# Optimization experiments

Measured on AMD Instinct MI355X. Metric: run time of the kernel, lower is better.

The kernel has to match this reference:

```python
import jax, jax.numpy as jnp
import numpy as np


def _safe_div(x, y):
    # avoid NaNs in branches that are masked out by jnp.where
    return x / jnp.where(jnp.abs(y) < 1e-12, 1.0, y)


def _closest_point_region(p, a, b, c):
    """Ericson closest-point-on-triangle, vectorized.
    p: [B,n,1,3]; a,b,c: [B,1,m,3] -> (dist2 [B,n,m], region [B,n,m] int32).
    Region codes: 0=vertA 1=vertB 2=vertC 3=edgeAB 4=edgeAC 5=edgeBC 6=face.
    """
    ab = b - a; ac = c - a; cb = c - b
    ap = p - a; bp = p - b; cp = p - c
    d1 = (ab * ap).sum(-1); d2 = (ac * ap).sum(-1)
    d3 = (ab * bp).sum(-1); d4 = (ac * bp).sum(-1)
    d5 = (ab * cp).sum(-1); d6 = (ac * cp).sum(-1)
    vc = d1 * d4 - d3 * d2
    vb = d5 * d2 - d1 * d6
    va = d3 * d6 - d5 * d4

    # candidate closest points per region
    v_ab = jnp.clip(_safe_div(d1, d1 - d3), 0.0, 1.0)
    v_ac = jnp.clip(_safe_div(d2, d2 - d6), 0.0, 1.0)
    v_bc = jnp.clip(_safe_div(d4 - d3, (d4 - d3) + (d5 - d6)), 0.0, 1.0)
    denom = va + vb + vc
    v_f = _safe_div(vb, denom); w_f = _safe_div(vc, denom)

    q_face = a + v_f[..., None] * ab + w_f[..., None] * ac
    q_ab = a + v_ab[..., None] * ab
    q_ac = a + v_ac[..., None] * ac
    q_bc = b + v_bc[..., None] * cb

    # region conditions (Ericson priority: a, b, ab, c, ac, bc, face)
    cond_a = (d1 <= 0) & (d2 <= 0)
    cond_b = (d3 >= 0) & (d4 <= d3)
    cond_ab = (vc <= 0) & (d1 >= 0) & (d3 <= 0)
    cond_c = (d6 >= 0) & (d5 <= d6)
    cond_ac = (vb <= 0) & (d2 >= 0) & (d6 <= 0)
    cond_bc = (va <= 0) & (d4 - d3 >= 0) & (d5 - d6 >= 0)

    def sel(cond, qc, code, q, region):
        q = jnp.where(cond[..., None], qc, q)
        region = jnp.where(cond, code, region)
        return q, region

    # apply lowest priority first so higher-priority regions overwrite
    q = q_face
    region = jnp.full(q.shape[:-1], 6, dtype=jnp.int32)
    q, region = sel(cond_bc, q_bc, 5, q, region)
    q, region = sel(cond_ac, q_ac, 4, q, region)
    q, region = sel(cond_c, c, 2, q, region)
    q, region = sel(cond_ab, q_ab, 3, q, region)
    q, region = sel(cond_b, b, 1, q, region)
    q, region = sel(cond_a, a, 0, q, region)

    diff = p - q
    dist2 = (diff * diff).sum(-1)  # squared distance, as in chamfer-style kernels
    return dist2, region


def setup_inputs() -> dict:
    key = jax.random.key(0)
    k1, k2, k3, k4 = jax.random.split(key, 4)
    B, n, m = 4, 4096, 512
    xyz1 = jax.random.normal(k1, (B, n, 3), dtype=jnp.float32)
    tri1 = jax.random.normal(k2, (B, m, 3), dtype=jnp.float32)
    tri2 = jax.random.normal(k3, (B, m, 3), dtype=jnp.float32)
    tri3 = jax.random.normal(k4, (B, m, 3), dtype=jnp.float32)
    return {"xyz1": xyz1, "tri1": tri1, "tri2": tri2, "tri3": tri3}


def reference(xyz1, tri1, tri2, tri3):
    p = xyz1[:, :, None, :]       # [B,n,1,3]
    a = tri1[:, None, :, :]       # [B,1,m,3]
    b = tri2[:, None, :, :]
    c = tri3[:, None, :, :]
    dist2, region = _closest_point_region(p, a, b, c)  # [B,n,m]
    index = jnp.argmin(dist2, axis=-1).astype(jnp.int32)            # [B,n]
    dist = jnp.min(dist2, axis=-1)                                  # [B,n]
    point = jnp.take_along_axis(region, index[..., None].astype(jnp.int64), axis=-1)[..., 0]
    return dist, point, index
```

## Files before the change

### kernel.cpp

```cpp
#include <hip/hip_runtime.h>
#include <math.h>

#define BB 4
#define NN 4096
#define MM 512
#define PTS 16
#define NPT 2
#define CHUNKS 32
#define MCHUNK (MM / CHUNKS)
#define TPB 512

__device__ __forceinline__ float safercp(float y) {
    float yy = (fabsf(y) < 1e-12f) ? 1.0f : y;
    return __builtin_amdgcn_rcpf(yy);
}

__device__ __forceinline__ float safediv(float x, float y) {
    float yy = (fabsf(y) < 1e-12f) ? 1.0f : y;
    return x / yy;
}

__device__ __forceinline__ float clip01(float x) {
    return fminf(fmaxf(x, 0.0f), 1.0f);
}

__device__ void exact_pair(float px, float py, float pz,
                           float ax, float ay, float az,
                           float bx, float by, float bz,
                           float cx, float cy, float cz,
                           float* dist2_out, int* reg_out) {
#pragma clang fp contract(off)
    const float abx = bx-ax, aby = by-ay, abz = bz-az;
    const float acx = cx-ax, acy = cy-ay, acz = cz-az;
    const float cbx = cx-bx, cby = cy-by, cbz = cz-bz;
    const float apx = px-ax, apy = py-ay, apz = pz-az;
    const float bpx = px-bx, bpy = py-by, bpz = pz-bz;
    const float cpx = px-cx, cpy = py-cy, cpz = pz-cz;

    const float d1 = abx*apx + aby*apy + abz*apz;
    const float d2 = acx*apx + acy*apy + acz*apz;
    const float d3 = abx*bpx + aby*bpy + abz*bpz;
    const float d4 = acx*bpx + acy*bpy + acz*bpz;
    const float d5 = abx*cpx + aby*cpy + abz*cpz;
    const float d6 = acx*cpx + acy*cpy + acz*cpz;

    const float vc = d1*d4 - d3*d2;
    const float vb = d5*d2 - d1*d6;
    const float va = d3*d6 - d5*d4;

    const float v_ab = clip01(safediv(d1, d1 - d3));
    const float v_ac = clip01(safediv(d2, d2 - d6));
    const float t43 = d4 - d3;
    const float t56 = d5 - d6;
    const float v_bc = clip01(safediv(t43, t43 + t56));
    const float denom = va + vb + vc;
    const float v_f = safediv(vb, denom);
    const float w_f = safediv(vc, denom);

    float qx = ax + v_f*abx + w_f*acx;
    float qy = ay + v_f*aby + w_f*acy;
    float qz = az + v_f*abz + w_f*acz;
    int reg = 6;
    const bool c_bc = (va <= 0.0f) && (t43 >= 0.0f) && (t56 >= 0.0f);
    if (c_bc) { qx = bx + v_bc*cbx; qy = by + v_bc*cby; qz = bz + v_bc*cbz; reg = 5; }
    const bool c_ac = (vb <= 0.0f) && (d2 >= 0.0f) && (d6 <= 0.0f);
    if (c_ac) { qx = ax + v_ac*acx; qy = ay + v_ac*acy; qz = az + v_ac*acz; reg = 4; }
    const bool c_c = (d6 >= 0.0f) && (d5 <= d6);
    if (c_c) { qx = cx; qy = cy; qz = cz; reg = 2; }
    const bool c_ab = (vc <= 0.0f) && (d1 >= 0.0f) && (d3 <= 0.0f);
    if (c_ab) { qx = ax + v_ab*abx; qy = ay + v_ab*aby; qz = az + v_ab*abz; reg = 3; }
    const bool c_b = (d3 >= 0.0f) && (d4 <= d3);
    if (c_b) { qx = bx; qy = by; qz = bz; reg = 1; }
    const bool c_a = (d1 <= 0.0f) && (d2 <= 0.0f);
    if (c_a) { qx = ax; qy = ay; qz = az; reg = 0; }

    const float dx = px - qx;
    const float dy = py - qy;
    const float dz = pz - qz;
    *dist2_out = dx*dx + dy*dy + dz*dz;
    *reg_out = reg;
}

__global__ __launch_bounds__(TPB) void tridist_kernel(
    const float* __restrict__ xyz1, const float* __restrict__ tri1,
    const float* __restrict__ tri2, const float* __restrict__ tri3,
    float* __restrict__ out)
{
    __shared__ float4 sT[MM * 7 + MM / 16];
    __shared__ float  sPd[NPT][128];
    __shared__ int    sPj[NPT][128];

    const int t  = threadIdx.x;
    const int b  = blockIdx.x >> 7;
    const int pb = blockIdx.x & 127;
    const int pt = t & (PTS - 1);
    const int ch = t >> 4;

    {
        const int jj = t;
        const float* g1 = tri1 + ((size_t)b * MM + jj) * 3;
        const float* g2 = tri2 + ((size_t)b * MM + jj) * 3;
        const float* g3 = tri3 + ((size_t)b * MM + jj) * 3;
        const float ax = g1[0], ay = g1[1], az = g1[2];
        const float bx = g2[0], by = g2[1], bz = g2[2];
        const float cx = g3[0], cy = g3[1], cz = g3[2];
        const float abx = bx-ax, aby = by-ay, abz = bz-az;
        const float acx = cx-ax, acy = cy-ay, acz = cz-az;
        const float cbx = cx-bx, cby = cy-by, cbz = cz-bz;
        const float aba  = fmaf(abz, az, fmaf(aby, ay, abx*ax));
        const float abb  = fmaf(abz, bz, fmaf(aby, by, abx*bx));
        const float abc_ = fmaf(abz, cz, fmaf(aby, cy, abx*cx));
        const float aca  = fmaf(acz, az, fmaf(acy, ay, acx*ax));
        const float acb_ = fmaf(acz, bz, fmaf(acy, by, acx*bx));
        const float acc_ = fmaf(acz, cz, fmaf(acy, cy, acx*cx));
        const float ab2  = fmaf(abz, abz, fmaf(aby, aby, abx*abx));
        const float ac2  = fmaf(acz, acz, fmaf(acy, acy, acx*acx));
        const float cb2  = fmaf(cbz, cbz, fmaf(cby, cby, cbx*cbx));
        const float abac = fmaf(abz, acz, fmaf(aby, acy, abx*acx));
        const float gdet = fmaf(ab2, ac2, -(abac*abac));
        const int base = jj * 7 + (jj >> 4);
        sT[base + 0] = make_float4(ax, ay, az, safercp(gdet));
        sT[base + 1] = make_float4(abx, aby, abz, safercp(ab2));
        sT[base + 2] = make_float4(acx, acy, acz, safercp(ac2));
        sT[base + 3] = make_float4(cbx, cby, cbz, safercp(cb2));
        sT[base + 4] = make_float4(aba, abb, abc_, cx);
        sT[base + 5] = make_float4(aca, acb_, acc_, cy);
        sT[base + 6] = make_float4(bx, by, bz, cz);
    }
    __syncthreads();

    float px[NPT], py[NPT], pz[NPT];
#pragma unroll
    for (int np = 0; np < NPT; ++np) {
        const int gi = b * NN + pb * 32 + np * PTS + pt;
        px[np] = xyz1[gi*3 + 0];
        py[np] = xyz1[gi*3 + 1];
        pz[np] = xyz1[gi*3 + 2];
    }

    float bestd[NPT] = {INFINITY, INFINITY};
    int   bestj[NPT] = {0, 0};

    for (int i = 0; i < MCHUNK; ++i) {
        const int j = ch * MCHUNK + i;
        const int base = j * 7 + ch;
        const float4 r0 = sT[base + 0];
        const float4 r1 = sT[base + 1];
        const float4 r2 = sT[base + 2];
        const float4 r3 = sT[base + 3];
        const float4 r4 = sT[base + 4];
        const float4 r5 = sT[base + 5];
        const float ax = r0.x, ay = r0.y, az = r0.z, rden = r0.w;
        const float abx = r1.x, aby = r1.y, abz = r1.z, rab2 = r1.w;
        const float acx = r2.x, acy = r2.y, acz = r2.z, rac2 = r2.w;
        const float cbx = r3.x, cby = r3.y, cbz = r3.z, rcb2 = r3.w;
        const float aba = r4.x, abb = r4.y, abc_ = r4.z;
        const float aca = r5.x, acb_ = r5.y, acc_ = r5.z;

#pragma unroll
        for (int np = 0; np < NPT; ++np) {
            const float s1 = fmaf(abz, pz[np], fmaf(aby, py[np], abx*px[np]));
            const float s2 = fmaf(acz, pz[np], fmaf(acy, py[np], acx*px[np]));
            const float d1 = s1 - aba, d3 = s1 - abb, d5 = s1 - abc_;
            const float d2 = s2 - aca, d4 = s2 - acb_, d6 = s2 - acc_;

            const float vc = fmaf(d1, d4, -(d3*d2));
            const float vb = fmaf(d5, d2, -(d1*d6));
            const float va = fmaf(d3, d6, -(d5*d4));
            const float t43 = d4 - d3;

            const float v_ab = clip01(d1 * rab2);
            const float v_ac = clip01(d2 * rac2);
            const float v_bc = clip01(t43 * rcb2);
            const float v_f = vb * rden;
            const float w_f = vc * rden;

            const float apx = px[np] - ax, apy = py[np] - ay, apz = pz[np] - az;
            const float bpx = apx - abx, bpy = apy - aby, bpz = apz - abz;

            float ex = fmaf(-v_ab, abx, apx), ey = fmaf(-v_ab, aby, apy), ez = fmaf(-v_ab, abz, apz);
            const float dAB = fmaf(ez, ez, fmaf(ey, ey, ex*ex));
            ex = fmaf(-v_ac, acx, apx); ey = fmaf(-v_ac, acy, apy); ez = fmaf(-v_ac, acz, apz);
            const float dAC = fmaf(ez, ez, fmaf(ey, ey, ex*ex));
            ex = fmaf(-v_bc, cbx, bpx); ey = fmaf(-v_bc, cby, bpy); ez = fmaf(-v_bc, cbz, bpz);
            const float dBC = fmaf(ez, ez, fmaf(ey, ey, ex*ex));
            ex = fmaf(-w_f, acx, fmaf(-v_f, abx, apx));
            ey = fmaf(-w_f, acy, fmaf(-v_f, aby, apy));
            ez = fmaf(-w_f, acz, fmaf(-v_f, abz, apz));
            const float dF = fmaf(ez, ez, fmaf(ey, ey, ex*ex));

            const bool inside = (va >= 0.0f) && (vb >= 0.0f) && (vc >= 0.0f);
            const float dseg = fminf(fminf(dAB, dAC), dBC);
            const float dist2 = inside ? dF : dseg;

            if (dist2 < bestd[np]) { bestd[np] = dist2; bestj[np] = j; }
        }
    }

#pragma unroll
    for (int np = 0; np < NPT; ++np) {
        for (int off = 16; off <= 32; off <<= 1) {
            const float od = __shfl_xor(bestd[np], off, 64);
            const int   oj = __shfl_xor(bestj[np], off, 64);
            if (od < bestd[np] || (od == bestd[np] && oj < bestj[np])) {
                bestd[np] = od; bestj[np] = oj;
            }
        }
    }
    const int lane = t & 63;
    const int w    = t >> 6;
    if (lane < PTS) {
#pragma unroll
        for (int np = 0; np < NPT; ++np) {
            sPd[np][w * PTS + lane] = bestd[np];
            sPj[np][w * PTS + lane] = bestj[np];
        }
    }
    __syncthreads();

    if (t < 32) {
        const int np = t >> 4;
        const int p  = t & 15;
        float bd = INFINITY; int bj = 0;
        for (int k = 0; k < 8; ++k) {
            const float dk = sPd[np][k * PTS + p];
            const int   jk = sPj[np][k * PTS + p];
            if (dk < bd || (dk == bd && jk < bj)) { bd = dk; bj = jk; }
        }
        const int base = bj * 7 + (bj >> 4);
        const float4 r0 = sT[base + 0];
        const float4 r4 = sT[base + 4];
        const float4 r5 = sT[base + 5];
        const float4 r6 = sT[base + 6];
        const int gidx = b * NN + pb * 32 + t;
        float dist2; int reg;
        exact_pair(xyz1[gidx*3+0], xyz1[gidx*3+1], xyz1[gidx*3+2],
                   r0.x, r0.y, r0.z,
                   r6.x, r6.y, r6.z,
                   r4.w, r5.w, r6.w,
                   &dist2, &reg);
        out[gidx]             = dist2;
        out[BB*NN + gidx]     = (float)reg;
        out[2*BB*NN + gidx]   = (float)bj;
    }
}

extern "C" void kernel_launch(void* const* d_in, const int* in_sizes, int n_in,
                              void* d_out, int out_size, void* d_ws, size_t ws_size,
                              hipStream_t stream) {
    const float* xyz1 = (const float*)d_in[0];
    const float* tri1 = (const float*)d_in[1];
    const float* tri2 = (const float*)d_in[2];
    const float* tri3 = (const float*)d_in[3];
    float* out = (float*)d_out;

    dim3 grid(BB * (NN / 32));
    dim3 block(TPB);
    tridist_kernel<<<grid, block, 0, stream>>>(xyz1, tri1, tri2, tri3, out);
}
```

Measured before the change: 74.25 us.

## Use plane-normal distance for face region and regroup points per thread

```diff
diff --git a/kernel.cpp b/kernel.cpp
--- a/kernel.cpp
+++ b/kernel.cpp
@@ -4,9 +4,9 @@
 #define BB 4
 #define NN 4096
 #define MM 512
-#define PTS 16
-#define NPT 2
-#define CHUNKS 32
+#define PTS 8
+#define NPT 4
+#define CHUNKS 64
 #define MCHUNK (MM / CHUNKS)
 #define TPB 512
 
@@ -86,15 +86,15 @@
     const float* __restrict__ tri2, const float* __restrict__ tri3,
     float* __restrict__ out)
 {
-    __shared__ float4 sT[MM * 7 + MM / 16];
-    __shared__ float  sPd[NPT][128];
-    __shared__ int    sPj[NPT][128];
+    __shared__ float4 sT[(MM / 8) * 49];
+    __shared__ float  sPd[NPT][64];
+    __shared__ int    sPj[NPT][64];
 
     const int t  = threadIdx.x;
     const int b  = blockIdx.x >> 7;
     const int pb = blockIdx.x & 127;
     const int pt = t & (PTS - 1);
-    const int ch = t >> 4;
+    const int ch = t >> 3;
 
     {
         const int jj = t;
@@ -108,24 +108,25 @@
         const float acx = cx-ax, acy = cy-ay, acz = cz-az;
         const float cbx = cx-bx, cby = cy-by, cbz = cz-bz;
         const float aba  = fmaf(abz, az, fmaf(aby, ay, abx*ax));
-        const float abb  = fmaf(abz, bz, fmaf(aby, by, abx*bx));
-        const float abc_ = fmaf(abz, cz, fmaf(aby, cy, abx*cx));
         const float aca  = fmaf(acz, az, fmaf(acy, ay, acx*ax));
-        const float acb_ = fmaf(acz, bz, fmaf(acy, by, acx*bx));
-        const float acc_ = fmaf(acz, cz, fmaf(acy, cy, acx*cx));
         const float ab2  = fmaf(abz, abz, fmaf(aby, aby, abx*abx));
         const float ac2  = fmaf(acz, acz, fmaf(acy, acy, acx*acx));
         const float cb2  = fmaf(cbz, cbz, fmaf(cby, cby, cbx*cbx));
         const float abac = fmaf(abz, acz, fmaf(aby, acy, abx*acx));
-        const float gdet = fmaf(ab2, ac2, -(abac*abac));
-        const int base = jj * 7 + (jj >> 4);
-        sT[base + 0] = make_float4(ax, ay, az, safercp(gdet));
+        const float nrx = fmaf(aby, acz, -(abz*acy));
+        const float nry = fmaf(abz, acx, -(abx*acz));
+        const float nrz = fmaf(abx, acy, -(aby*acx));
+        const float n2  = fmaf(nrz, nrz, fmaf(nry, nry, nrx*nrx));
+        const float rn  = __builtin_amdgcn_rsqf(fmaxf(n2, 1e-30f));
+        const float nx = nrx*rn, ny = nry*rn, nz = nrz*rn;
+        const float nna = -fmaf(nz, az, fmaf(ny, ay, nx*ax));
+        const int base = (jj >> 3) * 49 + (jj & 7) * 6;
+        sT[base + 0] = make_float4(ax, ay, az, nna);
         sT[base + 1] = make_float4(abx, aby, abz, safercp(ab2));
         sT[base + 2] = make_float4(acx, acy, acz, safercp(ac2));
         sT[base + 3] = make_float4(cbx, cby, cbz, safercp(cb2));
-        sT[base + 4] = make_float4(aba, abb, abc_, cx);
-        sT[base + 5] = make_float4(aca, acb_, acc_, cy);
-        sT[base + 6] = make_float4(bx, by, bz, cz);
+        sT[base + 4] = make_float4(nx, ny, nz, abac);
+        sT[base + 5] = make_float4(-aba, -aca, ab2, ac2);
     }
     __syncthreads();
 
@@ -138,31 +139,34 @@
         pz[np] = xyz1[gi*3 + 2];
     }
 
-    float bestd[NPT] = {INFINITY, INFINITY};
-    int   bestj[NPT] = {0, 0};
+    float bestd[NPT] = {INFINITY, INFINITY, INFINITY, INFINITY};
+    int   bestj[NPT] = {0, 0, 0, 0};
 
     for (int i = 0; i < MCHUNK; ++i) {
         const int j = ch * MCHUNK + i;
-        const int base = j * 7 + ch;
+        const int base = ch * 49 + i * 6;
         const float4 r0 = sT[base + 0];
         const float4 r1 = sT[base + 1];
         const float4 r2 = sT[base + 2];
         const float4 r3 = sT[base + 3];
         const float4 r4 = sT[base + 4];
         const float4 r5 = sT[base + 5];
-        const float ax = r0.x, ay = r0.y, az = r0.z, rden = r0.w;
+        const float ax = r0.x, ay = r0.y, az = r0.z, nna = r0.w;
         const float abx = r1.x, aby = r1.y, abz = r1.z, rab2 = r1.w;
         const float acx = r2.x, acy = r2.y, acz = r2.z, rac2 = r2.w;
         const float cbx = r3.x, cby = r3.y, cbz = r3.z, rcb2 = r3.w;
-        const float aba = r4.x, abb = r4.y, abc_ = r4.z;
-        const float aca = r5.x, acb_ = r5.y, acc_ = r5.z;
+        const float nx = r4.x, ny = r4.y, nz = r4.z, abac = r4.w;
+        const float naba = r5.x, naca = r5.y, ab2 = r5.z, ac2 = r5.w;
 
 #pragma unroll
         for (int np = 0; np < NPT; ++np) {
-            const float s1 = fmaf(abz, pz[np], fmaf(aby, py[np], abx*px[np]));
-            const float s2 = fmaf(acz, pz[np], fmaf(acy, py[np], acx*px[np]));
-            const float d1 = s1 - aba, d3 = s1 - abb, d5 = s1 - abc_;
-            const float d2 = s2 - aca, d4 = s2 - acb_, d6 = s2 - acc_;
+            const float d1 = fmaf(abz, pz[np], fmaf(aby, py[np], fmaf(abx, px[np], naba)));
+            const float d2 = fmaf(acz, pz[np], fmaf(acy, py[np], fmaf(acx, px[np], naca)));
+            const float h  = fmaf(nz,  pz[np], fmaf(ny,  py[np], fmaf(nx,  px[np], nna)));
+            const float d3 = d1 - ab2;
+            const float d4 = d2 - abac;
+            const float d5 = d1 - abac;
+            const float d6 = d2 - ac2;
 
             const float vc = fmaf(d1, d4, -(d3*d2));
             const float vb = fmaf(d5, d2, -(d1*d6));
@@ -172,8 +176,6 @@
             const float v_ab = clip01(d1 * rab2);
             const float v_ac = clip01(d2 * rac2);
             const float v_bc = clip01(t43 * rcb2);
-            const float v_f = vb * rden;
-            const float w_f = vc * rden;
 
             const float apx = px[np] - ax, apy = py[np] - ay, apz = pz[np] - az;
             const float bpx = apx - abx, bpy = apy - aby, bpz = apz - abz;
@@ -184,14 +186,11 @@
             const float dAC = fmaf(ez, ez, fmaf(ey, ey, ex*ex));
             ex = fmaf(-v_bc, cbx, bpx); ey = fmaf(-v_bc, cby, bpy); ez = fmaf(-v_bc, cbz, bpz);
             const float dBC = fmaf(ez, ez, fmaf(ey, ey, ex*ex));
-            ex = fmaf(-w_f, acx, fmaf(-v_f, abx, apx));
-            ey = fmaf(-w_f, acy, fmaf(-v_f, aby, apy));
-            ez = fmaf(-w_f, acz, fmaf(-v_f, abz, apz));
-            const float dF = fmaf(ez, ez, fmaf(ey, ey, ex*ex));
-
-            const bool inside = (va >= 0.0f) && (vb >= 0.0f) && (vc >= 0.0f);
+            const float dF = h * h;
+
+            const float mv = fminf(fminf(va, vb), vc);
             const float dseg = fminf(fminf(dAB, dAC), dBC);
-            const float dist2 = inside ? dF : dseg;
+            const float dist2 = (mv >= 0.0f) ? dF : dseg;
 
             if (dist2 < bestd[np]) { bestd[np] = dist2; bestj[np] = j; }
         }
@@ -199,7 +198,7 @@
 
 #pragma unroll
     for (int np = 0; np < NPT; ++np) {
-        for (int off = 16; off <= 32; off <<= 1) {
+        for (int off = 8; off <= 32; off <<= 1) {
             const float od = __shfl_xor(bestd[np], off, 64);
             const int   oj = __shfl_xor(bestj[np], off, 64);
             if (od < bestd[np] || (od == bestd[np] && oj < bestj[np])) {
@@ -219,25 +218,23 @@
     __syncthreads();
 
     if (t < 32) {
-        const int np = t >> 4;
-        const int p  = t & 15;
+        const int np = t >> 3;
+        const int p  = t & 7;
         float bd = INFINITY; int bj = 0;
         for (int k = 0; k < 8; ++k) {
             const float dk = sPd[np][k * PTS + p];
             const int   jk = sPj[np][k * PTS + p];
             if (dk < bd || (dk == bd && jk < bj)) { bd = dk; bj = jk; }
         }
-        const int base = bj * 7 + (bj >> 4);
-        const float4 r0 = sT[base + 0];
-        const float4 r4 = sT[base + 4];
-        const float4 r5 = sT[base + 5];
-        const float4 r6 = sT[base + 6];
+        const float* g1 = tri1 + ((size_t)b * MM + bj) * 3;
+        const float* g2 = tri2 + ((size_t)b * MM + bj) * 3;
+        const float* g3 = tri3 + ((size_t)b * MM + bj) * 3;
         const int gidx = b * NN + pb * 32 + t;
         float dist2; int reg;
         exact_pair(xyz1[gidx*3+0], xyz1[gidx*3+1], xyz1[gidx*3+2],
-                   r0.x, r0.y, r0.z,
-                   r6.x, r6.y, r6.z,
-                   r4.w, r5.w, r6.w,
+                   g1[0], g1[1], g1[2],
+                   g2[0], g2[1], g2[2],
+                   g3[0], g3[1], g3[2],
                    &dist2, &reg);
         out[gidx]             = dist2;
         out[BB*NN + gidx]     = (float)reg;
```

Measured after the change: 73.54 us. About the same (-1.0%).
